# Kernel tuning notes

Measured on AMD Instinct MI355X. Metric: run time of the kernel, lower is better.

Reference implementation:

```python
import jax, jax.numpy as jnp
import numpy as np

FS = 64          # feature_size for phi=0
A = 9            # anchors per location
NC = 80          # num classes
NHEAD = 3        # 3 + phi//3 head conv layers
K = 1000         # NMS candidate cap (fixed size for jit)
IOU_THR = 0.5
SCORE_THR = 0.05
BN_EPS = 4e-5
WEPS = 1e-4      # BiFPN fusion-weight epsilon


def conv(x, w, b, stride=1, pad=0):
    y = jax.lax.conv_general_dilated(x, w, (stride, stride), [(pad, pad), (pad, pad)],
                                     dimension_numbers=('NCHW', 'OIHW', 'NCHW'))
    return y + b[None, :, None, None]


def bnorm(x, g, bt, m, v):
    inv = jax.lax.rsqrt(v + BN_EPS)
    return (x - m[None, :, None, None]) * (g * inv)[None, :, None, None] + bt[None, :, None, None]


def up2(x):   # F.interpolate(scale_factor=2, mode='nearest')
    return jnp.repeat(jnp.repeat(x, 2, axis=2), 2, axis=3)


def down2(x):  # F.interpolate(scale_factor=0.5, mode='nearest') -> takes every 2nd pixel
    return x[:, :, ::2, ::2]


def run_head(x, ws, bs, ow, ob):
    for i in range(NHEAD):
        x = jax.nn.relu(conv(x, ws[i], bs[i], pad=1))
    return conv(x, ow, ob, pad=1)


def make_anchors(img_size):
    # standard retinanet-style anchors: levels 3..7, ratios {0.5,1,2}, scales {2^0,2^(1/3),2^(2/3)}
    ratios = np.array([0.5, 1.0, 2.0])
    scales = np.array([2 ** 0, 2 ** (1.0 / 3), 2 ** (2.0 / 3)])
    out = []
    for lvl in range(3, 8):
        stride = 2 ** lvl
        base = 2 ** (lvl + 2)
        s = np.tile(scales, len(ratios))
        r = np.repeat(ratios, len(scales))
        w = base * s
        areas = w * w
        w = np.sqrt(areas / r)
        h = w * r
        banch = np.stack([-w / 2, -h / 2, w / 2, h / 2], 1)  # [9,4] centered
        fs = img_size // stride
        sx = (np.arange(fs) + 0.5) * stride
        X, Y = np.meshgrid(sx, sx)
        shifts = np.stack([X.ravel(), Y.ravel(), X.ravel(), Y.ravel()], 1)
        out.append((shifts[:, None, :] + banch[None]).reshape(-1, 4))
    return jnp.asarray(np.concatenate(out, 0), jnp.float32)


def decode_boxes(anchors, reg, img_size):
    # BBoxTransform (mean 0, std [0.1,0.1,0.2,0.2]) followed by ClipBoxes
    wa = anchors[:, 2] - anchors[:, 0]
    ha = anchors[:, 3] - anchors[:, 1]
    cxa = anchors[:, 0] + 0.5 * wa
    cya = anchors[:, 1] + 0.5 * ha
    cx = cxa + reg[..., 0] * 0.1 * wa
    cy = cya + reg[..., 1] * 0.1 * ha
    w = jnp.exp(reg[..., 2] * 0.2) * wa
    h = jnp.exp(reg[..., 3] * 0.2) * ha
    x1 = jnp.maximum(cx - 0.5 * w, 0.0)
    y1 = jnp.maximum(cy - 0.5 * h, 0.0)
    x2 = jnp.minimum(cx + 0.5 * w, float(img_size))
    y2 = jnp.minimum(cy + 0.5 * h, float(img_size))
    return jnp.stack([x1, y1, x2, y2], -1)


def nms_keep(boxes, valid):
    # greedy IoU-threshold NMS over score-sorted boxes [K,4]; returns keep mask [K]
    x1, y1, x2, y2 = boxes[:, 0], boxes[:, 1], boxes[:, 2], boxes[:, 3]
    area = jnp.maximum(x2 - x1, 0.0) * jnp.maximum(y2 - y1, 0.0)
    iw = jnp.maximum(jnp.minimum(x2[:, None], x2[None, :]) - jnp.maximum(x1[:, None], x1[None, :]), 0.0)
    ih = jnp.maximum(jnp.minimum(y2[:, None], y2[None, :]) - jnp.maximum(y1[:, None], y1[None, :]), 0.0)
    inter = iw * ih
    iou = inter / (area[:, None] + area[None, :] - inter + 1e-8)
    idx = jnp.arange(boxes.shape[0])
    def body(i, keep):
        sup = keep[i] & (iou[i] > IOU_THR) & (idx > i)
        return keep & (~sup)
    return jax.lax.fori_loop(0, boxes.shape[0], body, valid)


def setup_inputs():
    key = jax.random.key(0)
    ks = iter(jax.random.split(key, 64))
    def wgt(shape, extra=1.0):
        fan = float(np.prod(shape[-3:]))
        return jax.random.normal(next(ks), shape, jnp.float32) * (extra / np.sqrt(fan))
    def bias(shape, scale=0.01):
        return jax.random.normal(next(ks), shape, jnp.float32) * scale
    inp = dict(
        c3=jax.random.normal(next(ks), (16, 40, 64, 64), jnp.float32),
        c4=jax.random.normal(next(ks), (16, 80, 32, 32), jnp.float32),
        c5=jax.random.normal(next(ks), (16, 192, 16, 16), jnp.float32),
        fpn_in_w3=wgt((FS, 40, 1, 1)), fpn_in_b3=bias((FS,)),
        fpn_in_w4=wgt((FS, 80, 1, 1)), fpn_in_b4=bias((FS,)),
        fpn_in_w5=wgt((FS, 192, 1, 1)), fpn_in_b5=bias((FS,)),
        fpn_in_w6=wgt((FS, 192, 3, 3)), fpn_in_b6=bias((FS,)),
        fpn_in_w7=wgt((FS, FS, 3, 3)), fpn_in_b7=bias((FS,)),
        fpn_td_w=wgt((2, 5, FS, FS, 1, 1)), fpn_td_b=bias((2, 5, FS)),
        fpn_td_gamma=1.0 + 0.05 * jax.random.normal(next(ks), (2, 5, FS), jnp.float32),
        fpn_td_beta=bias((2, 5, FS)),
        fpn_td_mean=bias((2, 5, FS), 0.1),
        fpn_td_var=0.75 + 0.5 * jax.random.uniform(next(ks), (2, 5, FS), jnp.float32),
        fpn_out_w=wgt((2, 5, FS, FS, 1, 1)), fpn_out_b=bias((2, 5, FS)),
        fpn_out_gamma=1.0 + 0.05 * jax.random.normal(next(ks), (2, 5, FS), jnp.float32),
        fpn_out_beta=bias((2, 5, FS)),
        fpn_out_mean=bias((2, 5, FS), 0.1),
        fpn_out_var=0.75 + 0.5 * jax.random.uniform(next(ks), (2, 5, FS), jnp.float32),
        fpn_w1=jax.random.uniform(next(ks), (2, 2), jnp.float32, 0.5, 1.5),
        fpn_w2=jax.random.uniform(next(ks), (2, 3), jnp.float32, 0.5, 1.5),
        cls_w=wgt((NHEAD, FS, FS, 3, 3)), cls_b=bias((NHEAD, FS)),
        cls_out_w=wgt((A * NC, FS, 3, 3)),
        cls_out_b=-2.0 + 0.5 * jax.random.normal(next(ks), (A * NC,), jnp.float32),
        reg_w=wgt((NHEAD, FS, FS, 3, 3)), reg_b=bias((NHEAD, FS)),
        reg_out_w=wgt((A * 4, FS, 3, 3), 0.1), reg_out_b=bias((A * 4,)),
        img_size=512,
    )
    return inp


def reference(c3, c4, c5, fpn_in_w3, fpn_in_b3, fpn_in_w4, fpn_in_b4, fpn_in_w5, fpn_in_b5,
              fpn_in_w6, fpn_in_b6, fpn_in_w7, fpn_in_b7, fpn_td_w, fpn_td_b, fpn_td_gamma,
              fpn_td_beta, fpn_td_mean, fpn_td_var, fpn_out_w, fpn_out_b, fpn_out_gamma,
              fpn_out_beta, fpn_out_mean, fpn_out_var, fpn_w1, fpn_w2, cls_w, cls_b,
              cls_out_w, cls_out_b, reg_w, reg_b, reg_out_w, reg_out_b, img_size):
    B = c3.shape[0]
    feats = None
    for blk in range(2):
        if blk == 0:
            p3 = conv(c3, fpn_in_w3, fpn_in_b3)
            p4 = conv(c4, fpn_in_w4, fpn_in_b4)
            p5 = conv(c5, fpn_in_w5, fpn_in_b5)
            p6 = conv(c5, fpn_in_w6, fpn_in_b6, stride=2, pad=1)
            p7 = conv(jax.nn.relu(p6), fpn_in_w7, fpn_in_b7, stride=2, pad=1)
            feats = [p3, p4, p5, p6, p7]
        p3x, p4x, p5x, p6x, p7x = feats
        w1 = jax.nn.relu(fpn_w1[blk]); w1 = w1 / (jnp.sum(w1) + WEPS)
        w2 = jax.nn.relu(fpn_w2[blk]); w2 = w2 / (jnp.sum(w2) + WEPS)
        td = lambda l, x: bnorm(conv(x, fpn_td_w[blk, l], fpn_td_b[blk, l]),
                                fpn_td_gamma[blk, l], fpn_td_beta[blk, l],
                                fpn_td_mean[blk, l], fpn_td_var[blk, l])
        oc = lambda l, x: bnorm(conv(x, fpn_out_w[blk, l], fpn_out_b[blk, l]),
                                fpn_out_gamma[blk, l], fpn_out_beta[blk, l],
                                fpn_out_mean[blk, l], fpn_out_var[blk, l])
        p7td = p7x
        p6td = td(3, w1[0] * p6x + w1[1] * up2(p7x))
        p5td = td(2, w1[0] * p5x + w1[1] * up2(p6x))
        p4td = td(1, w1[0] * p4x + w1[1] * up2(p5x))
        p3td = td(0, w1[0] * p3x + w1[1] * up2(p4x))
        p7o = oc(4, w2[0] * p7x + w2[1] * p7td + w2[2] * down2(p6td))
        p6o = oc(3, w2[0] * p6x + w2[1] * p6td + w2[2] * down2(p5td))
        p5o = oc(2, w2[0] * p5x + w2[1] * p5td + w2[2] * down2(p4td))
        p4o = oc(1, w2[0] * p4x + w2[1] * p4td + w2[2] * down2(p3td))
        feats = [p3td, p4o, p5o, p6o, p7o]
    regs, clss = [], []
    for f in feats:
        r = run_head(f, reg_w, reg_b, reg_out_w, reg_out_b)
        regs.append(r.transpose(0, 2, 3, 1).reshape(B, -1, 4))
        c = jax.nn.sigmoid(run_head(f, cls_w, cls_b, cls_out_w, cls_out_b))
        clss.append(c.transpose(0, 2, 3, 1).reshape(B, -1, NC))
    regression = jnp.concatenate(regs, 1)        # [B, N, 4]
    classification = jnp.concatenate(clss, 1)    # [B, N, NC]
    anchors = make_anchors(int(img_size))
    boxes = decode_boxes(anchors, regression, int(img_size))  # [B, N, 4]
    scores = jnp.max(classification, axis=2)     # [B, N]
    labels = jnp.argmax(classification, axis=2)  # [B, N]
    # eval path: image 0, threshold 0.05, greedy NMS @ IoU 0.5 (fixed-size top-K)
    s0, l0, b0 = scores[0], labels[0], boxes[0]
    masked = jnp.where(s0 > SCORE_THR, s0, -1.0)
    top_s, top_i = jax.lax.top_k(masked, K)
    top_b = b0[top_i]
    top_l = l0[top_i]
    valid = top_s > SCORE_THR
    keep = nms_keep(jax.lax.stop_gradient(top_b), valid)
    nms_scores = jnp.where(keep, top_s, 0.0)
    nms_labels = jnp.where(keep, top_l, -1).astype(jnp.int32)
    nms_boxes = jnp.where(keep[:, None], top_b, 0.0)
    return nms_scores, nms_labels, nms_boxes
```

## Files before the change

### kernel.cpp

```cpp
#include <hip/hip_runtime.h>

#define P_TOT 5456
#define NANCH 49104
#define KTOP 1000
#define CAND_CAP 2048

typedef unsigned long long u64;
typedef unsigned int u32;


__device__ __forceinline__ void level_of(int p, int& l, int& off, int& W, int& sh) {
  if (p < 4096)      { l = 0; off = 0;    W = 64; sh = 6; }
  else if (p < 5120) { l = 1; off = 4096; W = 32; sh = 5; }
  else if (p < 5376) { l = 2; off = 5120; W = 16; sh = 4; }
  else if (p < 5440) { l = 3; off = 5376; W = 8;  sh = 3; }
  else               { l = 4; off = 5440; W = 4;  sh = 2; }
}

__global__ void k_prep(const float* __restrict__ clsw, const float* __restrict__ regw,
                       const float* __restrict__ clsow, const float* __restrict__ regow,
                       float* __restrict__ RWc, float* __restrict__ RWr,
                       float* __restrict__ RWco, float* __restrict__ RWro,
                       u32* __restrict__ zhist, float* __restrict__ A, float* __restrict__ Bb,
                       float* __restrict__ Cb, float* __restrict__ Db) {
  int idx = blockIdx.x * 256 + threadIdx.x;
  if (idx < 656640) {
    const float* src; float* dst; int OC, local;
    if (idx < 110592)      { src = clsw;  dst = RWc;  OC = 64;  local = idx; }
    else if (idx < 221184) { src = regw;  dst = RWr;  OC = 64;  local = idx - 110592; }
    else if (idx < 635904) { src = clsow; dst = RWco; OC = 720; local = idx - 221184; }
    else                   { src = regow; dst = RWro; OC = 36;  local = idx - 635904; }
    int per = OC * 576;
    int layer = local / per;
    int rem = local - layer * per;
    int oc = rem / 576;
    int r2 = rem - oc * 576;
    int c = r2 / 9;
    int k = r2 - c * 9;
    dst[layer * per + (k * OC + oc) * 64 + c] = src[local];
    return;
  }
  int z = idx - 656640;
  if (z < 131136) { zhist[z] = 0; return; }
  z -= 131136;
  if (z < 16384) {
    float* buf = (z < 4096) ? A : (z < 8192) ? Bb : (z < 12288) ? Cb : Db;
    buf[86 * 4096 + (z & 4095)] = 0.f;
    return;
  }
  z -= 16384;
  if (z < 1024) RWro[20736 + z] = 0.f;
}

__global__ void k_fpn_in(const float* __restrict__ c3, const float* __restrict__ w3, const float* __restrict__ b3,
                         const float* __restrict__ c4i, const float* __restrict__ w4, const float* __restrict__ b4,
                         const float* __restrict__ c5, const float* __restrict__ w5, const float* __restrict__ b5,
                         const float* __restrict__ w6, const float* __restrict__ b6,
                         float* __restrict__ F, float4* __restrict__ F4) {
  int bx = blockIdx.x;
  if (bx < 320) {
    const float* x; const float* w; const float* b; int Cin, npix, off, c4o, p;
    if (bx < 256) { x = c3; w = w3; b = b3; Cin = 40; npix = 4096; off = 0;
                    c4o = bx >> 4; p = (bx & 15) * 256 + threadIdx.x; }
    else          { int lo = bx - 256; x = c4i; w = w4; b = b4; Cin = 80; npix = 1024; off = 4096;
                    c4o = lo >> 2; p = (lo & 3) * 256 + threadIdx.x; }
    int oc4 = c4o * 4;
    float acc[4] = {0.f,0.f,0.f,0.f};
    for (int c = 0; c < Cin; ++c) {
      float xv = x[c * npix + p];
#pragma unroll
      for (int o = 0; o < 4; ++o)
        acc[o] = fmaf(w[(oc4 + o) * Cin + c], xv, acc[o]);
    }
    int px = off + p;
    float4 r;
    r.x = acc[0] + b[oc4 + 0]; r.y = acc[1] + b[oc4 + 1];
    r.z = acc[2] + b[oc4 + 2]; r.w = acc[3] + b[oc4 + 3];
    F4[((px >> 6) << 10) + (c4o << 6) + (px & 63)] = r;
  } else if (bx < 384) {
    int oc = bx - 320;
    int p = threadIdx.x;
    float acc = 0.f;
    for (int c = 0; c < 192; ++c)
      acc = fmaf(w5[oc * 192 + c], c5[c * 256 + p], acc);
    int px = 5120 + p;
    F[((px >> 6) << 12) + ((oc >> 2) << 8) + ((px & 63) << 2) + (oc & 3)] = acc + b5[oc];
  } else {
    int oc = bx - 384;
    int tid = threadIdx.x;
    int cg = tid >> 6, pix = tid & 63;
    int oy = pix >> 3, ox = pix & 7;
    float acc = 0.f;
    int c0 = cg * 48;
    for (int c = c0; c < c0 + 48; ++c) {
      const float* xc = c5 + c * 256;
      const float* wc = w6 + (oc * 192 + c) * 9;
#pragma unroll
      for (int ky = 0; ky < 3; ++ky) {
        int iy = oy * 2 + ky - 1;
        if ((unsigned)iy >= 16u) continue;
#pragma unroll
        for (int kx = 0; kx < 3; ++kx) {
          int ix = ox * 2 + kx - 1;
          if ((unsigned)ix >= 16u) continue;
          acc = fmaf(wc[ky * 3 + kx], xc[iy * 16 + ix], acc);
        }
      }
    }
    __shared__ float red[4][64];
    red[cg][pix] = acc;
    __syncthreads();
    if (cg == 0) {
      float s = red[0][pix] + red[1][pix] + red[2][pix] + red[3][pix] + b6[oc];
      F[(84 << 12) + ((oc >> 2) << 8) + (pix << 2) + (oc & 3)] = s;
    }
  }
}

__global__ void k_conv_p7(const float* __restrict__ w, const float* __restrict__ b,
                          float* __restrict__ F) {
  int oc = blockIdx.x;
  int t = threadIdx.x;
  int cg = t >> 4, pix = t & 15;
  int oy = pix >> 2, ox = pix & 3;
  float acc = 0.f;
  int c0 = cg * 16;
  for (int c = c0; c < c0 + 16; ++c) {
#pragma unroll
    for (int ky = 0; ky < 3; ++ky) {
      int iy = oy * 2 + ky - 1;
      if ((unsigned)iy >= 8u) continue;
#pragma unroll
      for (int kx = 0; kx < 3; ++kx) {
        int ix = ox * 2 + kx - 1;
        if ((unsigned)ix >= 8u) continue;
        float xv = fmaxf(F[(84 << 12) + ((c >> 2) << 8) + ((iy * 8 + ix) << 2) + (c & 3)], 0.f);
        acc = fmaf(w[(oc * 64 + c) * 9 + ky * 3 + kx], xv, acc);
      }
    }
  }
  acc += __shfl_down(acc, 32);
  acc += __shfl_down(acc, 16);
  if (cg == 0)
    F[(85 << 12) + ((oc >> 2) << 8) + (pix << 2) + (oc & 3)] = acc + b[oc];
}

__global__ __launch_bounds__(256) void k_td_t(const float4* __restrict__ F4, float4* __restrict__ TD4,
                     const float* __restrict__ tw, const float* __restrict__ tb,
                     const float* __restrict__ tg, const float* __restrict__ tbt,
                     const float* __restrict__ tm, const float* __restrict__ tv,
                     const float* __restrict__ w1raw, int blk) {
  int bx = blockIdx.x, S = bx * 64;
  int l, off, W, sh; level_of(S, l, off, W, sh);
  int tid = threadIdx.x;
  if (l == 4) {
    if (blockIdx.y == 0) {
      int pxrel = tid >> 4, c4 = tid & 15;
      TD4[(85 << 10) + (c4 << 6) + pxrel] = F4[(85 << 10) + (c4 << 6) + pxrel];
    }
    return;
  }
  __shared__ float part[3][8][64];
  float wav = fmaxf(w1raw[blk * 2 + 0], 0.f);
  float wbv = fmaxf(w1raw[blk * 2 + 1], 0.f);
  float s = wav + wbv + 1e-4f;
  wav /= s; wbv /= s;
  int lane = tid & 63;
  int kh = __builtin_amdgcn_readfirstlane(tid >> 6);
  int g = blockIdx.y;
  int ocb = g * 8;
  int px = S + lane;
  int loc = px - off, yy = loc >> sh, xx = loc & (W - 1);
  int Wu = W >> 1;
  int pup = off + W * W + (yy >> 1) * Wu + (xx >> 1);
  int c4base = kh * 4;
  int fup = ((pup >> 6) << 10) + (pup & 63) + (c4base << 6);
  int fself = (bx << 10) + lane + (c4base << 6);
  float acc[8] = {};
  const float4* wt4 = (const float4*)tw + (size_t)((blk * 5 + l) * 64) * 16 + c4base;
#pragma unroll
  for (int c4 = 0; c4 < 4; ++c4) {
    float4 a = F4[fself + (c4 << 6)];
    float4 b = F4[fup + (c4 << 6)];
    float4 fin;
    fin.x = wav * a.x + wbv * b.x; fin.y = wav * a.y + wbv * b.y;
    fin.z = wav * a.z + wbv * b.z; fin.w = wav * a.w + wbv * b.w;
#pragma unroll
    for (int o = 0; o < 8; ++o) {
      float4 wv = wt4[(ocb + o) * 16 + c4];
      acc[o] = fmaf(fin.x, wv.x, fmaf(fin.y, wv.y, fmaf(fin.z, wv.z, fmaf(fin.w, wv.w, acc[o]))));
    }
  }
  if (kh) {
#pragma unroll
    for (int o = 0; o < 8; ++o) part[kh - 1][o][lane] = acc[o];
  }
  __syncthreads();
  if (kh) return;
#pragma unroll
  for (int o = 0; o < 8; ++o)
    acc[o] += part[0][o][lane] + part[1][o][lane] + part[2][o][lane];
  int idxbase = (blk * 5 + l) * 64 + ocb;
#pragma unroll
  for (int q = 0; q < 2; ++q) {
    float r[4];
#pragma unroll
    for (int j = 0; j < 4; ++j) {
      int o = q * 4 + j, idx = idxbase + o;
      float xv = acc[o] + tb[idx];
      float inv = 1.0f / sqrtf(tv[idx] + 4e-5f);
      r[j] = (xv - tm[idx]) * (tg[idx] * inv) + tbt[idx];
    }
    float4 rq; rq.x = r[0]; rq.y = r[1]; rq.z = r[2]; rq.w = r[3];
    TD4[(bx << 10) + (((ocb >> 2) + q) << 6) + lane] = rq;
  }
}

__global__ __launch_bounds__(256) void k_out_t(const float4* __restrict__ F4, const float4* __restrict__ TD4,
                      float4* __restrict__ OUT4,
                      const float* __restrict__ ow, const float* __restrict__ ob,
                      const float* __restrict__ og, const float* __restrict__ obt,
                      const float* __restrict__ om, const float* __restrict__ ov,
                      const float* __restrict__ w2raw, int blk) {
  int bx = blockIdx.x, S = bx * 64;
  int l, off, W, sh; level_of(S, l, off, W, sh);
  int tid = threadIdx.x;
  if (l == 0) {
    if (blockIdx.y == 0)
      for (int j = tid; j < 1024; j += 256)
        OUT4[(bx << 10) + j] = TD4[(bx << 10) + j];
    return;
  }
  __shared__ float part[3][8][64];
  float wav = fmaxf(w2raw[blk * 3 + 0], 0.f);
  float wbv = fmaxf(w2raw[blk * 3 + 1], 0.f);
  float wcv = fmaxf(w2raw[blk * 3 + 2], 0.f);
  float s = wav + wbv + wcv + 1e-4f;
  wav /= s; wbv /= s; wcv /= s;
  int lane = tid & 63;
  int kh = __builtin_amdgcn_readfirstlane(tid >> 6);
  int g = blockIdx.y;
  int ocb = g * 8;
  int px = S + lane;
  bool pxok = px < P_TOT;
  int loc = px - off, yy = loc >> sh, xx = loc & (W - 1);
  int Wd = W << 1;
  int offd = off - Wd * Wd;
  int pdn = offd + (2 * yy) * Wd + 2 * xx;
  int c4base = kh * 4;
  int fself = (bx << 10) + lane + (c4base << 6);
  int fdn = (pxok ? (((pdn >> 6) << 10) + (pdn & 63)) : ((bx << 10) + lane)) + (c4base << 6);
  float acc[8] = {};
  const float4* wt4 = (const float4*)ow + (size_t)((blk * 5 + l) * 64) * 16 + c4base;
#pragma unroll
  for (int c4 = 0; c4 < 4; ++c4) {
    float4 a = F4[fself + (c4 << 6)];
    float4 b = TD4[fself + (c4 << 6)];
    float4 c = TD4[fdn + (c4 << 6)];
    float4 fin;
    fin.x = wav * a.x + wbv * b.x + wcv * c.x;
    fin.y = wav * a.y + wbv * b.y + wcv * c.y;
    fin.z = wav * a.z + wbv * b.z + wcv * c.z;
    fin.w = wav * a.w + wbv * b.w + wcv * c.w;
#pragma unroll
    for (int o = 0; o < 8; ++o) {
      float4 wv = wt4[(ocb + o) * 16 + c4];
      acc[o] = fmaf(fin.x, wv.x, fmaf(fin.y, wv.y, fmaf(fin.z, wv.z, fmaf(fin.w, wv.w, acc[o]))));
    }
  }
  if (kh) {
#pragma unroll
    for (int o = 0; o < 8; ++o) part[kh - 1][o][lane] = acc[o];
  }
  __syncthreads();
  if (kh || !pxok) return;
#pragma unroll
  for (int o = 0; o < 8; ++o)
    acc[o] += part[0][o][lane] + part[1][o][lane] + part[2][o][lane];
  int idxbase = (blk * 5 + l) * 64 + ocb;
#pragma unroll
  for (int q = 0; q < 2; ++q) {
    float r[4];
#pragma unroll
    for (int j = 0; j < 4; ++j) {
      int o = q * 4 + j, idx = idxbase + o;
      float xv = acc[o] + ob[idx];
      float inv = 1.0f / sqrtf(ov[idx] + 4e-5f);
      r[j] = (xv - om[idx]) * (og[idx] * inv) + obt[idx];
    }
    float4 rq; rq.x = r[0]; rq.y = r[1]; rq.z = r[2]; rq.w = r[3];
    OUT4[(bx << 10) + (((ocb >> 2) + q) << 6) + lane] = rq;
  }
}

__device__ __forceinline__ void tap_idx(int px, int off, int W, int sh, int fidx[9]) {
  int loc = px - off, y = loc >> sh, x = loc & (W - 1);
  int zb = (86 << 10) + (px & 63);
#pragma unroll
  for (int ky = 0; ky < 3; ++ky)
#pragma unroll
    for (int kx = 0; kx < 3; ++kx) {
      int iy = y + ky - 1, ix = x + kx - 1;
      bool v = ((unsigned)iy < (unsigned)W) && ((unsigned)ix < (unsigned)W);
      int pp = px + (ky - 1) * W + (kx - 1);
      fidx[ky * 3 + kx] = v ? (((pp >> 6) << 10) + (pp & 63)) : zb;
    }
}

__global__ __launch_bounds__(256) void k_conv3m(const float4* __restrict__ Fr, const float4* __restrict__ Fc,
                        float4* __restrict__ Or, float4* __restrict__ Oc,
                        const float* __restrict__ RWr, const float* __restrict__ RWc,
                        const float* __restrict__ br, const float* __restrict__ bc) {
  __shared__ float part[3][8][64];
  int S = blockIdx.x * 64;
  int l, off, W, sh; level_of(S, l, off, W, sh);
  int lane = threadIdx.x & 63;
  int kh = __builtin_amdgcn_readfirstlane(threadIdx.x >> 6);
  int g = blockIdx.y;
  const float4* X; float4* O; const float* RW; const float* bias; int ocb;
  if (g < 8) { X = Fr; O = Or; RW = RWr; bias = br; ocb = g * 8; }
  else       { X = Fc; O = Oc; RW = RWc; bias = bc; ocb = (g - 8) * 8; }
  int px = S + lane;
  int fidx[9];
  tap_idx(px, off, W, sh, fidx);
  float acc[8];
#pragma unroll
  for (int o = 0; o < 8; ++o) acc[o] = 0.f;
  int c4base = kh * 4;
  const float4* W4 = (const float4*)RW + c4base;
#pragma unroll
  for (int t = 0; t < 9; ++t) {
    const float4* wb = W4 + (size_t)(t * 64 + ocb) * 16;
    int fi = fidx[t] + (c4base << 6);
#pragma unroll
    for (int c4 = 0; c4 < 4; ++c4) {
      float4 xv = X[fi + (c4 << 6)];
#pragma unroll
      for (int o = 0; o < 8; ++o) {
        float4 wv = wb[o * 16 + c4];
        acc[o] = fmaf(xv.x, wv.x, fmaf(xv.y, wv.y, fmaf(xv.z, wv.z, fmaf(xv.w, wv.w, acc[o]))));
      }
    }
  }
  if (kh) {
#pragma unroll
    for (int o = 0; o < 8; ++o) part[kh - 1][o][lane] = acc[o];
  }
  __syncthreads();
  if (kh || px >= P_TOT) return;
#pragma unroll
  for (int o = 0; o < 8; ++o)
    acc[o] += part[0][o][lane] + part[1][o][lane] + part[2][o][lane];
#pragma unroll
  for (int q = 0; q < 2; ++q) {
    float4 r;
    r.x = fmaxf(acc[q*4+0] + bias[ocb+q*4+0], 0.f);
    r.y = fmaxf(acc[q*4+1] + bias[ocb+q*4+1], 0.f);
    r.z = fmaxf(acc[q*4+2] + bias[ocb+q*4+2], 0.f);
    r.w = fmaxf(acc[q*4+3] + bias[ocb+q*4+3], 0.f);
    O[(blockIdx.x << 10) + (((ocb >> 2) + q) << 6) + lane] = r;
  }
}

__global__ __launch_bounds__(256) void k_conv3c(const float4* __restrict__ Fc, const float4* __restrict__ Fr,
                        const float* __restrict__ RWc, const float* __restrict__ bc,
                        const float* __restrict__ RWr, const float* __restrict__ br,
                        u64* __restrict__ pamax, float* __restrict__ REGb) {
  __shared__ float part[2][8][128];
  int lane = threadIdx.x & 63;
  int wid = __builtin_amdgcn_readfirstlane(threadIdx.x >> 6);
  int gp = wid >> 1, kh = wid & 1;
  int g = blockIdx.y * 2 + gp;
  bool is_cls = g < 90;
  bool is_reg = (g >= 90) && (g < 95);
  int ocb, OCw; const float4* W4; const float4* F4;
  if (is_reg) { ocb = (g - 90) * 8; OCw = 36; W4 = (const float4*)RWr; F4 = Fr; }
  else        { ocb = is_cls ? g * 8 : 0; OCw = 720; W4 = (const float4*)RWc; F4 = Fc; }
  int S = blockIdx.x * 128;
  int px1 = S + lane;
  int px2 = S + 64 + lane;
  bool ok2 = px2 < P_TOT;
  int l, off, W, sh;
  level_of(px1, l, off, W, sh);
  int f1[9];
  tap_idx(px1, off, W, sh, f1);
  int f2[9];
  if (ok2) {
    int l2, off2, W2, sh2;
    level_of(px2, l2, off2, W2, sh2);
    tap_idx(px2, off2, W2, sh2, f2);
  } else {
    int zb = (86 << 10) + lane;
#pragma unroll
    for (int t = 0; t < 9; ++t) f2[t] = zb;
  }
  float a1[8], a2[8];
#pragma unroll
  for (int o = 0; o < 8; ++o) { a1[o] = 0.f; a2[o] = 0.f; }
  int c4base = kh * 8;
  const float4* W4b = W4 + c4base;
#pragma unroll
  for (int t = 0; t < 9; ++t) {
    const float4* wb = W4b + (size_t)(t * OCw + ocb) * 16;
    int fi1 = f1[t] + (c4base << 6), fi2 = f2[t] + (c4base << 6);
#pragma unroll 4
    for (int c4 = 0; c4 < 8; ++c4) {
      float4 x1 = F4[fi1 + (c4 << 6)];
      float4 x2 = F4[fi2 + (c4 << 6)];
#pragma unroll
      for (int o = 0; o < 8; ++o) {
        float4 wv = wb[o * 16 + c4];
        a1[o] = fmaf(x1.x, wv.x, fmaf(x1.y, wv.y, fmaf(x1.z, wv.z, fmaf(x1.w, wv.w, a1[o]))));
        a2[o] = fmaf(x2.x, wv.x, fmaf(x2.y, wv.y, fmaf(x2.z, wv.z, fmaf(x2.w, wv.w, a2[o]))));
      }
    }
  }
  if (kh) {
#pragma unroll
    for (int o = 0; o < 8; ++o) {
      part[gp][o][lane] = a1[o];
      part[gp][o][64 + lane] = a2[o];
    }
  }
  __syncthreads();
  if (kh) return;
#pragma unroll
  for (int o = 0; o < 8; ++o) {
    a1[o] += part[gp][o][lane];
    a2[o] += part[gp][o][64 + lane];
  }
  if (is_cls) {
    int a0 = ocb / 80;
    int cls0 = ocb - a0 * 80;
    u64 k1 = 0ULL, k2 = 0ULL;
#pragma unroll
    for (int o = 0; o < 8; ++o) {
      float bi = bc[ocb + o];
      int cls = cls0 + o;
      u32 low = (u32)(127 - cls);
      float v1 = a1[o] + bi;
      u32 b1 = __float_as_uint(v1);
      b1 = (b1 & 0x80000000u) ? ~b1 : (b1 | 0x80000000u);
      u64 key1 = ((u64)b1 << 32) | low;
      k1 = k1 > key1 ? k1 : key1;
      float v2 = a2[o] + bi;
      u32 b2 = __float_as_uint(v2);
      b2 = (b2 & 0x80000000u) ? ~b2 : (b2 | 0x80000000u);
      u64 key2 = ((u64)b2 << 32) | low;
      k2 = k2 > key2 ? k2 : key2;
    }
    pamax[g * 5504 + px1] = k1;
    if (ok2) pamax[g * 5504 + px2] = k2;
  } else if (is_reg) {
    int nv = (g == 94) ? 4 : 8;
    for (int o = 0; o < nv; ++o) {
      int oc = ocb + o;
      float v1 = a1[o] + br[oc];
      REGb[((size_t)(px1 >> 6) * 9 + (oc >> 2)) * 256 + (px1 & 63) * 4 + (oc & 3)] = v1;
      if (ok2) {
        float v2 = a2[o] + br[oc];
        REGb[((size_t)(px2 >> 6) * 9 + (oc >> 2)) * 256 + (px2 & 63) * 4 + (oc & 3)] = v2;
      }
    }
  }
}

__global__ void k_decode_score(const float4* __restrict__ REG4, const u64* __restrict__ pamax,
                               float* __restrict__ score, int* __restrict__ label,
                               float* __restrict__ boxes, u32* __restrict__ ukey,
                               u32* __restrict__ hist1) {
  int aid = blockIdx.x * 256 + threadIdx.x;
  if (aid >= NANCH) return;
  int p = aid / 9;
  int a = aid - p * 9;
  int l, off, W, sh; level_of(p, l, off, W, sh);
  int loc = p - off, y = loc >> sh, x = loc & (W - 1);
  int s_idx = a % 3, r_idx = a / 3;
  double scale = (s_idx == 0) ? 1.0 : ((s_idx == 1) ? 1.2599210498948732 : 1.5874010519681994);
  double ratio = (r_idx == 0) ? 0.5 : ((r_idx == 1) ? 1.0 : 2.0);
  double strided = (double)(8 << l);
  double based = (double)(32 << l);
  double w0 = based * scale;
  double wA = sqrt(w0 * w0 / ratio);
  double hA = wA * ratio;
  double cxd = (x + 0.5) * strided;
  double cyd = (y + 0.5) * strided;
  float ax1 = (float)(cxd - wA / 2.0);
  float ay1 = (float)(cyd - hA / 2.0);
  float ax2 = (float)(cxd + wA / 2.0);
  float ay2 = (float)(cyd + hA / 2.0);
  float wa = ax2 - ax1, ha = ay2 - ay1;
  float cxa = ax1 + 0.5f * wa, cya = ay1 + 0.5f * ha;
  int blk = p >> 6, pxin = p & 63;
  float4 rq = REG4[blk * 576 + (a << 6) + pxin];
  float ncx = cxa + (rq.x * 0.1f) * wa;
  float ncy = cya + (rq.y * 0.1f) * ha;
  float nw = expf(rq.z * 0.2f) * wa;
  float nh = expf(rq.w * 0.2f) * ha;
  float bx1 = fmaxf(ncx - 0.5f * nw, 0.f);
  float by1 = fmaxf(ncy - 0.5f * nh, 0.f);
  float bx2 = fminf(ncx + 0.5f * nw, 512.f);
  float by2 = fminf(ncy + 0.5f * nh, 512.f);
  boxes[aid * 4 + 0] = bx1; boxes[aid * 4 + 1] = by1;
  boxes[aid * 4 + 2] = bx2; boxes[aid * 4 + 3] = by2;
  u64 key = 0ULL;
  const u64* pa = pamax + (size_t)(a * 10) * 5504 + p;
#pragma unroll
  for (int gi = 0; gi < 10; ++gi) {
    u64 k = pa[gi * 5504];
    key = key > k ? key : k;
  }
  u32 b = (u32)(key >> 32);
  b = (b & 0x80000000u) ? (b & 0x7FFFFFFFu) : ~b;
  float best = __uint_as_float(b);
  int bl = 127 - (int)(key & 0xFFFFFFFFu);
  float sc = 1.f / (1.f + expf(-best));
  score[aid] = sc; label[aid] = bl;
  u32 u = 0u;
  if (sc > 0.05f) u = __float_as_uint(sc) | 0x80000000u;
  ukey[aid] = u;
  if (u) atomicAdd(&hist1[u >> 16], 1u);
}

__global__ __launch_bounds__(1024) void k_scanA(const u32* __restrict__ hist, u32* __restrict__ ctrl) {
  __shared__ u32 cs[1024];
  __shared__ u32 suf[1024];
  int t = threadIdx.x;
  u32 s = 0;
  int base = t * 64;
  for (int b = 0; b < 64; ++b) s += hist[base + b];
  cs[t] = s;
  suf[t] = s;
  __syncthreads();
  for (int d = 1; d < 1024; d <<= 1) {
    u32 v = (t + d < 1024) ? suf[t + d] : 0u;
    __syncthreads();
    suf[t] += v;
    __syncthreads();
  }
  u32 total = suf[0];
  if (total < (u32)KTOP) {
    if (t == 0) { ctrl[0] = 0x20000u; ctrl[1] = total; ctrl[2] = 1u; }
    return;
  }
  u32 excl = suf[t] - cs[t];
  if (excl < (u32)KTOP && excl + cs[t] >= (u32)KTOP) {
    u32 c2 = excl; int B1 = t * 64; u32 hB1 = 0;
    for (int b = t * 64 + 63; b >= t * 64; --b) {
      u32 h = hist[b];
      if (c2 + h >= (u32)KTOP) { B1 = b; hB1 = h; break; }
      c2 += h;
    }
    ctrl[0] = (u32)B1; ctrl[1] = c2;
    if (c2 + hB1 <= (u32)CAND_CAP) {
      ctrl[2] = (u32)B1 << 16;
      ctrl[5] = 1u;
    }
  }
}

__global__ void k_histB(const u32* __restrict__ ukey, u32* __restrict__ hist2,
                        const u32* __restrict__ ctrl) {
  if (ctrl[5]) return;
  int aid = blockIdx.x * 256 + threadIdx.x;
  if (aid >= NANCH) return;
  u32 u = ukey[aid];
  if (u && (u >> 16) == ctrl[0]) atomicAdd(&hist2[u & 0xFFFFu], 1u);
}

__global__ __launch_bounds__(1024) void k_scanB(const u32* __restrict__ hist, u32* __restrict__ ctrl) {
  if (ctrl[0] > 0xFFFFu || ctrl[5]) return;
  __shared__ u32 cs[1024];
  u32 s = 0;
  int base = threadIdx.x * 64;
  for (int b = 0; b < 64; ++b) s += hist[base + b];
  cs[threadIdx.x] = s;
  __syncthreads();
  if (threadIdx.x == 0) {
    u32 CA = ctrl[1];
    u32 cum = CA; int cc = -1;
    for (int tt = 1023; tt >= 0; --tt) {
      if (cum + cs[tt] >= (u32)KTOP) { cc = tt; break; }
      cum += cs[tt];
    }
    u32 B2 = 0;
    if (cc >= 0) {
      for (int b = cc * 64 + 63; b >= cc * 64; --b) {
        u32 h = hist[b];
        if (cum + h >= (u32)KTOP) { B2 = (u32)b; break; }
        cum += h;
      }
    }
    ctrl[2] = (ctrl[0] << 16) | B2;
  }
}

__global__ void k_compact(const u32* __restrict__ ukey, u64* __restrict__ cand,
                          u32* __restrict__ ctrl) {
  int aid = blockIdx.x * 256 + threadIdx.x;
  if (aid >= NANCH) return;
  u32 u = ukey[aid];
  u32 T = ctrl[2];
  if (u >= T && u != 0) {
    u32 pos = atomicAdd(&ctrl[3], 1u);
    if (pos < (u32)CAND_CAP)
      cand[pos] = (((u64)u) << 32) | (u32)(~(u32)aid);
  }
}

__global__ __launch_bounds__(256) void k_rank(const u64* __restrict__ cand, u32* __restrict__ ctrl,
                                              const int* __restrict__ label,
                                              const float* __restrict__ boxes,
                                              float* __restrict__ tops, int* __restrict__ topl,
                                              float* __restrict__ topb) {
  __shared__ u64 key[CAND_CAP];
  int C = min((int)ctrl[3], CAND_CAP);
  for (int i = threadIdx.x; i < C; i += 256) key[i] = cand[i];
  __syncthreads();
  int i = blockIdx.x * 256 + threadIdx.x;
  if (i < C) {
    u64 ki = key[i];
    int rank = 0;
    for (int j = 0; j < C; ++j) rank += (key[j] > ki) ? 1 : 0;
    if (rank < KTOP) {
      u32 u = (u32)(ki >> 32);
      int aid = (int)(~((u32)ki));
      tops[rank] = __uint_as_float(u & 0x7FFFFFFFu);
      topl[rank] = label[aid];
      topb[rank * 4 + 0] = boxes[aid * 4 + 0];
      topb[rank * 4 + 1] = boxes[aid * 4 + 1];
      topb[rank * 4 + 2] = boxes[aid * 4 + 2];
      topb[rank * 4 + 3] = boxes[aid * 4 + 3];
    }
  }
  if (blockIdx.x == 0) {
    for (int r = threadIdx.x; r < KTOP; r += 256) {
      if (r >= C) {
        tops[r] = -1.f; topl[r] = -1;
        topb[r * 4 + 0] = 0.f; topb[r * 4 + 1] = 0.f;
        topb[r * 4 + 2] = 0.f; topb[r * 4 + 3] = 0.f;
      }
    }
    if (threadIdx.x == 0) ctrl[4] = (u32)min(C, KTOP);
  }
}

__global__ void k_iou(const float* __restrict__ topb, const u32* __restrict__ ctrl,
                      u64* __restrict__ mask) {
  int wid = threadIdx.x >> 6, lane = threadIdx.x & 63;
  int i = blockIdx.x * 4 + wid;
  int V = (int)ctrl[4];
  if (i >= V) return;
  float x1i = topb[i * 4], y1i = topb[i * 4 + 1], x2i = topb[i * 4 + 2], y2i = topb[i * 4 + 3];
  float ai = fmaxf(x2i - x1i, 0.f) * fmaxf(y2i - y1i, 0.f);
  int w0 = i >> 6;
  if (lane == 0)
    for (int w = 0; w < w0; ++w) mask[i * 16 + w] = 0ULL;
  for (int w = w0; w < 16; ++w) {
    int j = w * 64 + lane;
    bool bit = false;
    if (j < KTOP && j > i) {
      float x1j = topb[j * 4], y1j = topb[j * 4 + 1], x2j = topb[j * 4 + 2], y2j = topb[j * 4 + 3];
      float aj = fmaxf(x2j - x1j, 0.f) * fmaxf(y2j - y1j, 0.f);
      float iw = fmaxf(fminf(x2i, x2j) - fmaxf(x1i, x1j), 0.f);
      float ih = fmaxf(fminf(y2i, y2j) - fmaxf(y1i, y1j), 0.f);
      float inter = iw * ih;
      float iou = inter / (ai + aj - inter + 1e-8f);
      bit = iou > 0.5f;
    }
    u64 m = __ballot(bit);
    if (lane == 0) mask[i * 16 + w] = m;
  }
}

__global__ __launch_bounds__(256) void k_nmsfinal(const u64* __restrict__ mask,
                                                  const float* __restrict__ tops,
                                                  const int* __restrict__ topl,
                                                  const float* __restrict__ topb,
                                                  float* __restrict__ out) {
  __shared__ char kf[KTOP];
  int tid = threadIdx.x;
  if (tid < 64) {
    const int la = tid;
    const int rg = la >> 4;
    const int wg = la & 15;
    u64 remw = 0ULL;

#define LOADB(b, upd, intra, vsc) do {                                   \
    int rb = (b) * 64;                                                   \
    _Pragma("unroll")                                                    \
    for (int k = 0; k < 16; ++k)                                         \
      upd[k] = mask[(u32)(rb + rg + 4 * k) * 16u + (u32)wg];             \
    intra = mask[(u32)(rb + la) * 16u + (u32)(b)];                       \
    vsc = tops[rb + la];                                                 \
  } while (0)

#define PROC(b, upd, intra, vsc) do {                                    \
    u64 validmask = __ballot((vsc) > 0.05f);                             \
    u32 ilo = (u32)(intra);                                              \
    u32 ihi = (u32)((intra) >> 32);                                      \
    u64 supmask = ((u64)__builtin_amdgcn_readlane((int)(remw >> 32), (b)) << 32) | \
                  (u32)__builtin_amdgcn_readlane((int)(u32)remw, (b));   \
    u64 keptmask = 0ULL;                                                 \
    for (int i = 0; i < 64; ++i) {                                       \
      u32 rlo = (u32)__builtin_amdgcn_readlane((int)ilo, i);             \
      u32 rhi = (u32)__builtin_amdgcn_readlane((int)ihi, i);             \
      u64 take = (u64)0 - (((validmask >> i) & 1ULL) & (~(supmask >> i) & 1ULL)); \
      keptmask |= (1ULL << i) & take;                                    \
      supmask |= (((u64)rhi << 32) | rlo) & take;                       \
    }                                                                    \
    u64 kk = keptmask >> rg;                                             \
    u64 acc = 0ULL;                                                      \
    _Pragma("unroll")                                                    \
    for (int k = 0; k < 16; ++k)                                         \
      if ((kk >> (4 * k)) & 1ULL) acc |= upd[k];                         \
    acc |= __shfl_xor(acc, 16);                                          \
    acc |= __shfl_xor(acc, 32);                                          \
    remw |= acc;                                                         \
    int j = (b) * 64 + la;                                               \
    if (j < KTOP) kf[j] = (char)((keptmask >> la) & 1ULL);               \
  } while (0)

    u64 updA[16], updB[16];
    u64 intraA, intraB;
    float vscA, vscB;
    LOADB(0, updA, intraA, vscA);
    for (int bb = 0; bb < 16; bb += 2) {
      if (bb + 1 < 16) LOADB(bb + 1, updB, intraB, vscB);
      PROC(bb, updA, intraA, vscA);
      if (bb + 2 < 16) LOADB(bb + 2, updA, intraA, vscA);
      if (bb + 1 < 16) PROC(bb + 1, updB, intraB, vscB);
    }
#undef LOADB
#undef PROC
  }
  __syncthreads();
  for (int r = tid; r < KTOP; r += 256) {
    int k = kf[r];
    out[r] = k ? tops[r] : 0.f;
    out[KTOP + r] = k ? (float)topl[r] : -1.f;
    out[2 * KTOP + r * 4 + 0] = k ? topb[r * 4 + 0] : 0.f;
    out[2 * KTOP + r * 4 + 1] = k ? topb[r * 4 + 1] : 0.f;
    out[2 * KTOP + r * 4 + 2] = k ? topb[r * 4 + 2] : 0.f;
    out[2 * KTOP + r * 4 + 3] = k ? topb[r * 4 + 3] : 0.f;
  }
}

extern "C" void kernel_launch(void* const* d_in, const int* in_sizes, int n_in,
                              void* d_out, int out_size, void* d_ws, size_t ws_size,
                              hipStream_t stream) {
  const float* c3    = (const float*)d_in[0];
  const float* c4i   = (const float*)d_in[1];
  const float* c5    = (const float*)d_in[2];
  const float* w3    = (const float*)d_in[3];  const float* b3 = (const float*)d_in[4];
  const float* w4    = (const float*)d_in[5];  const float* b4 = (const float*)d_in[6];
  const float* w5    = (const float*)d_in[7];  const float* b5 = (const float*)d_in[8];
  const float* w6    = (const float*)d_in[9];  const float* b6 = (const float*)d_in[10];
  const float* w7    = (const float*)d_in[11]; const float* b7 = (const float*)d_in[12];
  const float* tdw   = (const float*)d_in[13]; const float* tdb  = (const float*)d_in[14];
  const float* tdg   = (const float*)d_in[15]; const float* tdbt = (const float*)d_in[16];
  const float* tdm   = (const float*)d_in[17]; const float* tdv  = (const float*)d_in[18];
  const float* ow    = (const float*)d_in[19]; const float* ob   = (const float*)d_in[20];
  const float* og    = (const float*)d_in[21]; const float* obt  = (const float*)d_in[22];
  const float* om    = (const float*)d_in[23]; const float* ov   = (const float*)d_in[24];
  const float* w1    = (const float*)d_in[25]; const float* w2   = (const float*)d_in[26];
  const float* clsw  = (const float*)d_in[27]; const float* clsb = (const float*)d_in[28];
  const float* clsow = (const float*)d_in[29]; const float* clsob= (const float*)d_in[30];
  const float* regw  = (const float*)d_in[31]; const float* regb = (const float*)d_in[32];
  const float* regow = (const float*)d_in[33]; const float* regob= (const float*)d_in[34];

  float* ws = (float*)d_ws;
  const size_t NF = 356352;
  float* A    = ws;
  float* Bb   = ws + NF;
  float* Cb   = ws + 2 * NF;
  float* Db   = ws + 3 * NF;
  float* RWc  = ws + 4 * NF;
  float* RWco = RWc + 110592;
  float* RWr  = RWco + 414720;
  float* RWro = RWr + 110592;
  float* REGb = RWro + 21760;
  u64*   pamax = (u64*)(REGb + 198144);
  float* scoreb = (float*)(pamax + 495360);
  int*   labelb = (int*)(scoreb + 49104);
  float* boxesb = (float*)(labelb + 49104);
  u32* hist1 = (u32*)(boxesb + 196416);
  u32* hist2 = hist1 + 65536;
  u32* ctrl  = hist2 + 65536;
  u64* cand  = (u64*)(ctrl + 64);
  float* tops = (float*)(cand + CAND_CAP);
  int*   topl = (int*)(tops + 1024);
  float* topb = (float*)(topl + 1024);
  u64*   mask = (u64*)(topb + 4096);
  u32*   ukeyb = (u32*)(mask + 16384);

  float4* A4 = (float4*)A; float4* B4 = (float4*)Bb;
  float4* C4 = (float4*)Cb; float4* D4 = (float4*)Db;
  float4* REG4 = (float4*)REGb;

  k_prep<<<dim3(3146), 256, 0, stream>>>(clsw, regw, clsow, regow, RWc, RWr, RWco, RWro,
                                         hist1, A, Bb, Cb, Db);

  k_fpn_in<<<dim3(448), 256, 0, stream>>>(c3, w3, b3, c4i, w4, b4, c5, w5, b5, w6, b6, A, A4);
  k_conv_p7<<<dim3(64), 64, 0, stream>>>(w7, b7, A);

  k_td_t<<<dim3(86, 8), 256, 0, stream>>>(A4, B4, tdw, tdb, tdg, tdbt, tdm, tdv, w1, 0);
  k_out_t<<<dim3(86, 8), 256, 0, stream>>>(A4, B4, C4, ow, ob, og, obt, om, ov, w2, 0);
  k_td_t<<<dim3(86, 8), 256, 0, stream>>>(C4, B4, tdw, tdb, tdg, tdbt, tdm, tdv, w1, 1);
  k_out_t<<<dim3(86, 8), 256, 0, stream>>>(C4, B4, A4, ow, ob, og, obt, om, ov, w2, 1);

  k_conv3m<<<dim3(86, 16), 256, 0, stream>>>(A4, A4, C4, D4, RWr, RWc, regb, clsb);
  k_conv3m<<<dim3(86, 16), 256, 0, stream>>>(C4, D4, B4, A4, RWr + 36864, RWc + 36864, regb + 64, clsb + 64);
  k_conv3m<<<dim3(86, 16), 256, 0, stream>>>(B4, A4, C4, D4, RWr + 73728, RWc + 73728, regb + 128, clsb + 128);
  k_conv3c<<<dim3(43, 48), 256, 0, stream>>>(D4, C4, RWco, clsob, RWro, regob, pamax, REGb);

  k_decode_score<<<dim3(192), 256, 0, stream>>>(REG4, pamax, scoreb, labelb, boxesb, ukeyb, hist1);
  k_scanA<<<dim3(1), 1024, 0, stream>>>(hist1, ctrl);
  k_histB<<<dim3(192), 256, 0, stream>>>(ukeyb, hist2, ctrl);
  k_scanB<<<dim3(1), 1024, 0, stream>>>(hist2, ctrl);
  k_compact<<<dim3(192), 256, 0, stream>>>(ukeyb, cand, ctrl);
  k_rank<<<dim3(CAND_CAP / 256), 256, 0, stream>>>(cand, ctrl, labelb, boxesb, tops, topl, topb);
  k_iou<<<dim3(250), 256, 0, stream>>>(topb, ctrl, mask);
  k_nmsfinal<<<dim3(1), 256, 0, stream>>>(mask, tops, topl, topb, (float*)d_out);
}
```

Measured before the change: 416.6 us.

## Merge FPN input convs into prep kernel and split conv3c reduction four ways

Folds the k_fpn_in blocks into k_prep as extra blocks, which saves one kernel launch. The two kernels are independent, because the weight reshuffles and buffer zeroing do not touch the rows of A that the FPN convs write. The final head conv k_conv3c now runs one output group per block with four waves, each taking a quarter of the channel dimension, instead of two groups per block with two waves each. The block count roughly doubles and the per-wave serial loop gets shorter, at the cost of a larger shared-memory reduction.

```diff
diff --git a/kernel.cpp b/kernel.cpp
--- a/kernel.cpp
+++ b/kernel.cpp
@@ -22,8 +22,76 @@
                        float* __restrict__ RWc, float* __restrict__ RWr,
                        float* __restrict__ RWco, float* __restrict__ RWro,
                        u32* __restrict__ zhist, float* __restrict__ A, float* __restrict__ Bb,
-                       float* __restrict__ Cb, float* __restrict__ Db) {
-  int idx = blockIdx.x * 256 + threadIdx.x;
+                       float* __restrict__ Cb, float* __restrict__ Db,
+                       const float* __restrict__ c3, const float* __restrict__ w3, const float* __restrict__ b3,
+                       const float* __restrict__ c4i, const float* __restrict__ w4, const float* __restrict__ b4,
+                       const float* __restrict__ c5, const float* __restrict__ w5, const float* __restrict__ b5,
+                       const float* __restrict__ w6, const float* __restrict__ b6) {
+  int bxg = blockIdx.x;
+  if (bxg >= 3146) {
+    int bx = bxg - 3146;
+    float4* F4 = (float4*)A;
+    float* F = A;
+    if (bx < 320) {
+      const float* x; const float* w; const float* b; int Cin, npix, off, c4o, p;
+      if (bx < 256) { x = c3; w = w3; b = b3; Cin = 40; npix = 4096; off = 0;
+                      c4o = bx >> 4; p = (bx & 15) * 256 + threadIdx.x; }
+      else          { int lo = bx - 256; x = c4i; w = w4; b = b4; Cin = 80; npix = 1024; off = 4096;
+                      c4o = lo >> 2; p = (lo & 3) * 256 + threadIdx.x; }
+      int oc4 = c4o * 4;
+      float acc[4] = {0.f,0.f,0.f,0.f};
+      for (int c = 0; c < Cin; ++c) {
+        float xv = x[c * npix + p];
+#pragma unroll
+        for (int o = 0; o < 4; ++o)
+          acc[o] = fmaf(w[(oc4 + o) * Cin + c], xv, acc[o]);
+      }
+      int px = off + p;
+      float4 r;
+      r.x = acc[0] + b[oc4 + 0]; r.y = acc[1] + b[oc4 + 1];
+      r.z = acc[2] + b[oc4 + 2]; r.w = acc[3] + b[oc4 + 3];
+      F4[((px >> 6) << 10) + (c4o << 6) + (px & 63)] = r;
+    } else if (bx < 384) {
+      int oc = bx - 320;
+      int p = threadIdx.x;
+      float acc = 0.f;
+      for (int c = 0; c < 192; ++c)
+        acc = fmaf(w5[oc * 192 + c], c5[c * 256 + p], acc);
+      int px = 5120 + p;
+      F[((px >> 6) << 12) + ((oc >> 2) << 8) + ((px & 63) << 2) + (oc & 3)] = acc + b5[oc];
+    } else {
+      int oc = bx - 384;
+      int tid = threadIdx.x;
+      int cg = tid >> 6, pix = tid & 63;
+      int oy = pix >> 3, ox = pix & 7;
+      float acc = 0.f;
+      int c0 = cg * 48;
+      for (int c = c0; c < c0 + 48; ++c) {
+        const float* xc = c5 + c * 256;
+        const float* wc = w6 + (oc * 192 + c) * 9;
+#pragma unroll
+        for (int ky = 0; ky < 3; ++ky) {
+          int iy = oy * 2 + ky - 1;
+          if ((unsigned)iy >= 16u) continue;
+#pragma unroll
+          for (int kx = 0; kx < 3; ++kx) {
+            int ix = ox * 2 + kx - 1;
+            if ((unsigned)ix >= 16u) continue;
+            acc = fmaf(wc[ky * 3 + kx], xc[iy * 16 + ix], acc);
+          }
+        }
+      }
+      __shared__ float red[4][64];
+      red[cg][pix] = acc;
+      __syncthreads();
+      if (cg == 0) {
+        float s = red[0][pix] + red[1][pix] + red[2][pix] + red[3][pix] + b6[oc];
+        F[(84 << 12) + ((oc >> 2) << 8) + (pix << 2) + (oc & 3)] = s;
+      }
+    }
+    return;
+  }
+  int idx = bxg * 256 + threadIdx.x;
   if (idx < 656640) {
     const float* src; float* dst; int OC, local;
     if (idx < 110592)      { src = clsw;  dst = RWc;  OC = 64;  local = idx; }
@@ -50,71 +118,6 @@
   }
   z -= 16384;
   if (z < 1024) RWro[20736 + z] = 0.f;
-}
-
-__global__ void k_fpn_in(const float* __restrict__ c3, const float* __restrict__ w3, const float* __restrict__ b3,
-                         const float* __restrict__ c4i, const float* __restrict__ w4, const float* __restrict__ b4,
-                         const float* __restrict__ c5, const float* __restrict__ w5, const float* __restrict__ b5,
-                         const float* __restrict__ w6, const float* __restrict__ b6,
-                         float* __restrict__ F, float4* __restrict__ F4) {
-  int bx = blockIdx.x;
-  if (bx < 320) {
-    const float* x; const float* w; const float* b; int Cin, npix, off, c4o, p;
-    if (bx < 256) { x = c3; w = w3; b = b3; Cin = 40; npix = 4096; off = 0;
-                    c4o = bx >> 4; p = (bx & 15) * 256 + threadIdx.x; }
-    else          { int lo = bx - 256; x = c4i; w = w4; b = b4; Cin = 80; npix = 1024; off = 4096;
-                    c4o = lo >> 2; p = (lo & 3) * 256 + threadIdx.x; }
-    int oc4 = c4o * 4;
-    float acc[4] = {0.f,0.f,0.f,0.f};
-    for (int c = 0; c < Cin; ++c) {
-      float xv = x[c * npix + p];
-#pragma unroll
-      for (int o = 0; o < 4; ++o)
-        acc[o] = fmaf(w[(oc4 + o) * Cin + c], xv, acc[o]);
-    }
-    int px = off + p;
-    float4 r;
-    r.x = acc[0] + b[oc4 + 0]; r.y = acc[1] + b[oc4 + 1];
-    r.z = acc[2] + b[oc4 + 2]; r.w = acc[3] + b[oc4 + 3];
-    F4[((px >> 6) << 10) + (c4o << 6) + (px & 63)] = r;
-  } else if (bx < 384) {
-    int oc = bx - 320;
-    int p = threadIdx.x;
-    float acc = 0.f;
-    for (int c = 0; c < 192; ++c)
-      acc = fmaf(w5[oc * 192 + c], c5[c * 256 + p], acc);
-    int px = 5120 + p;
-    F[((px >> 6) << 12) + ((oc >> 2) << 8) + ((px & 63) << 2) + (oc & 3)] = acc + b5[oc];
-  } else {
-    int oc = bx - 384;
-    int tid = threadIdx.x;
-    int cg = tid >> 6, pix = tid & 63;
-    int oy = pix >> 3, ox = pix & 7;
-    float acc = 0.f;
-    int c0 = cg * 48;
-    for (int c = c0; c < c0 + 48; ++c) {
-      const float* xc = c5 + c * 256;
-      const float* wc = w6 + (oc * 192 + c) * 9;
-#pragma unroll
-      for (int ky = 0; ky < 3; ++ky) {
-        int iy = oy * 2 + ky - 1;
-        if ((unsigned)iy >= 16u) continue;
-#pragma unroll
-        for (int kx = 0; kx < 3; ++kx) {
-          int ix = ox * 2 + kx - 1;
-          if ((unsigned)ix >= 16u) continue;
-          acc = fmaf(wc[ky * 3 + kx], xc[iy * 16 + ix], acc);
-        }
-      }
-    }
-    __shared__ float red[4][64];
-    red[cg][pix] = acc;
-    __syncthreads();
-    if (cg == 0) {
-      float s = red[0][pix] + red[1][pix] + red[2][pix] + red[3][pix] + b6[oc];
-      F[(84 << 12) + ((oc >> 2) << 8) + (pix << 2) + (oc & 3)] = s;
-    }
-  }
 }
 
 __global__ void k_conv_p7(const float* __restrict__ w, const float* __restrict__ b,
@@ -366,16 +369,14 @@
                         const float* __restrict__ RWc, const float* __restrict__ bc,
                         const float* __restrict__ RWr, const float* __restrict__ br,
                         u64* __restrict__ pamax, float* __restrict__ REGb) {
-  __shared__ float part[2][8][128];
+  __shared__ float part[3][8][128];
   int lane = threadIdx.x & 63;
-  int wid = __builtin_amdgcn_readfirstlane(threadIdx.x >> 6);
-  int gp = wid >> 1, kh = wid & 1;
-  int g = blockIdx.y * 2 + gp;
+  int kh = __builtin_amdgcn_readfirstlane(threadIdx.x >> 6);
+  int g = blockIdx.y;
   bool is_cls = g < 90;
-  bool is_reg = (g >= 90) && (g < 95);
   int ocb, OCw; const float4* W4; const float4* F4;
-  if (is_reg) { ocb = (g - 90) * 8; OCw = 36; W4 = (const float4*)RWr; F4 = Fr; }
-  else        { ocb = is_cls ? g * 8 : 0; OCw = 720; W4 = (const float4*)RWc; F4 = Fc; }
+  if (is_cls) { ocb = g * 8; OCw = 720; W4 = (const float4*)RWc; F4 = Fc; }
+  else        { ocb = (g - 90) * 8; OCw = 36; W4 = (const float4*)RWr; F4 = Fr; }
   int S = blockIdx.x * 128;
   int px1 = S + lane;
   int px2 = S + 64 + lane;
@@ -397,14 +398,14 @@
   float a1[8], a2[8];
 #pragma unroll
   for (int o = 0; o < 8; ++o) { a1[o] = 0.f; a2[o] = 0.f; }
-  int c4base = kh * 8;
+  int c4base = kh * 4;
   const float4* W4b = W4 + c4base;
 #pragma unroll
   for (int t = 0; t < 9; ++t) {
     const float4* wb = W4b + (size_t)(t * OCw + ocb) * 16;
     int fi1 = f1[t] + (c4base << 6), fi2 = f2[t] + (c4base << 6);
-#pragma unroll 4
-    for (int c4 = 0; c4 < 8; ++c4) {
+#pragma unroll
+    for (int c4 = 0; c4 < 4; ++c4) {
       float4 x1 = F4[fi1 + (c4 << 6)];
       float4 x2 = F4[fi2 + (c4 << 6)];
 #pragma unroll
@@ -418,16 +419,16 @@
   if (kh) {
 #pragma unroll
     for (int o = 0; o < 8; ++o) {
-      part[gp][o][lane] = a1[o];
-      part[gp][o][64 + lane] = a2[o];
+      part[kh - 1][o][lane] = a1[o];
+      part[kh - 1][o][64 + lane] = a2[o];
     }
   }
   __syncthreads();
   if (kh) return;
 #pragma unroll
   for (int o = 0; o < 8; ++o) {
-    a1[o] += part[gp][o][lane];
-    a2[o] += part[gp][o][64 + lane];
+    a1[o] += part[0][o][lane] + part[1][o][lane] + part[2][o][lane];
+    a2[o] += part[0][o][64 + lane] + part[1][o][64 + lane] + part[2][o][64 + lane];
   }
   if (is_cls) {
     int a0 = ocb / 80;
@@ -451,7 +452,7 @@
     }
     pamax[g * 5504 + px1] = k1;
     if (ok2) pamax[g * 5504 + px2] = k2;
-  } else if (is_reg) {
+  } else {
     int nv = (g == 94) ? 4 : 8;
     for (int o = 0; o < nv; ++o) {
       int oc = ocb + o;
@@ -798,10 +799,9 @@
   float4* C4 = (float4*)Cb; float4* D4 = (float4*)Db;
   float4* REG4 = (float4*)REGb;
 
-  k_prep<<<dim3(3146), 256, 0, stream>>>(clsw, regw, clsow, regow, RWc, RWr, RWco, RWro,
-                                         hist1, A, Bb, Cb, Db);
-
-  k_fpn_in<<<dim3(448), 256, 0, stream>>>(c3, w3, b3, c4i, w4, b4, c5, w5, b5, w6, b6, A, A4);
+  k_prep<<<dim3(3594), 256, 0, stream>>>(clsw, regw, clsow, regow, RWc, RWr, RWco, RWro,
+                                         hist1, A, Bb, Cb, Db,
+                                         c3, w3, b3, c4i, w4, b4, c5, w5, b5, w6, b6);
   k_conv_p7<<<dim3(64), 64, 0, stream>>>(w7, b7, A);
 
   k_td_t<<<dim3(86, 8), 256, 0, stream>>>(A4, B4, tdw, tdb, tdg, tdbt, tdm, tdv, w1, 0);
@@ -812,7 +812,7 @@
   k_conv3m<<<dim3(86, 16), 256, 0, stream>>>(A4, A4, C4, D4, RWr, RWc, regb, clsb);
   k_conv3m<<<dim3(86, 16), 256, 0, stream>>>(C4, D4, B4, A4, RWr + 36864, RWc + 36864, regb + 64, clsb + 64);
   k_conv3m<<<dim3(86, 16), 256, 0, stream>>>(B4, A4, C4, D4, RWr + 73728, RWc + 73728, regb + 128, clsb + 128);
-  k_conv3c<<<dim3(43, 48), 256, 0, stream>>>(D4, C4, RWco, clsob, RWro, regob, pamax, REGb);
+  k_conv3c<<<dim3(43, 95), 256, 0, stream>>>(D4, C4, RWco, clsob, RWro, regob, pamax, REGb);
 
   k_decode_score<<<dim3(192), 256, 0, stream>>>(REG4, pamax, scoreb, labelb, boxesb, ukeyb, hist1);
   k_scanA<<<dim3(1), 1024, 0, stream>>>(hist1, ctrl);
```

Result: slower. 630.5 us (+51.3%).
